# Kernel tuning notes

Hardware: AMD Instinct MI355X
Metric: run time of the kernel (lower is better)

Reference implementation:

```python
import jax, jax.numpy as jnp
import numpy as np

B, T, D = 4, 2048, 1024
H = 16
HD = D // H


def setup_inputs() -> dict:
    key = jax.random.key(0)
    ks = jax.random.split(key, 9)
    s = 1.0 / np.sqrt(D)
    return {
        "x": jax.random.normal(ks[0], (B, T, D), dtype=jnp.float32),
        "Wk": jax.random.normal(ks[1], (D, D), dtype=jnp.float32) * s,
        "bk": jnp.zeros((D,), dtype=jnp.float32),
        "Wq": jax.random.normal(ks[2], (D, D), dtype=jnp.float32) * s,
        "bq": jnp.zeros((D,), dtype=jnp.float32),
        "Wv": jax.random.normal(ks[3], (D, D), dtype=jnp.float32) * s,
        "bv": jnp.zeros((D,), dtype=jnp.float32),
        "Wp": jax.random.normal(ks[4], (D, D), dtype=jnp.float32) * s,
        "bp": jnp.zeros((D,), dtype=jnp.float32),
    }


def reference(x, Wk, bk, Wq, bq, Wv, bv, Wp, bp):
    Bv, Tv, Dv = x.shape
    # project and split heads: [B, H, T, HD]
    def heads(w, b):
        return (x @ w + b).reshape(Bv, Tv, H, HD).transpose(0, 2, 1, 3)
    k = heads(Wk, bk)
    q = heads(Wq, bq)
    v = heads(Wv, bv)
    scale = 1.0 / np.sqrt(HD)
    att = jnp.einsum('bhqd,bhkd->bhqk', q, k) * scale  # [B,H,T,T]
    causal = jnp.tril(jnp.ones((Tv, Tv), dtype=bool))
    att = jnp.where(causal[None, None, :, :], att, -jnp.inf)
    att = jax.nn.softmax(att, axis=-1)
    y = jnp.einsum('bhqk,bhkd->bhqd', att, v)  # [B,H,T,HD]
    y = y.transpose(0, 2, 1, 3).reshape(Bv, Tv, Dv)
    return y @ Wp + bp
```

## Files before the change

kernel.cpp:

```cpp
#include <hip/hip_runtime.h>
#include <stdint.h>

#define Bb 4
#define Tt 2048
#define Dd 1024
#define Hh 16
#define HDd 64
#define Mm 8192

typedef __attribute__((ext_vector_type(8))) short bf16x8;
typedef __attribute__((ext_vector_type(4))) float f32x4;
typedef __attribute__((ext_vector_type(16))) float f32x16;

#define MFMA(a, b, c) __builtin_amdgcn_mfma_f32_16x16x32_bf16(a, b, c, 0, 0, 0)
#define MFMA32(a, b, c) __builtin_amdgcn_mfma_f32_32x32x16_bf16(a, b, c, 0, 0, 0)

#define LOG2E 1.44269504088896340736f
#if __has_builtin(__builtin_amdgcn_exp2f)
#define EXP2(x) __builtin_amdgcn_exp2f(x)
#else
#define EXP2(x) __expf((x) * 0.69314718055994530942f)
#endif

union vfu { uint2 u2[2]; bf16x8 v; };
union apu { uint32_t u[4]; bf16x8 v; };

__device__ __forceinline__ unsigned short f2b(float f) {
  union { float f; uint32_t u; } v; v.f = f;
  return (unsigned short)((v.u + 0x7FFFu + ((v.u >> 16) & 1u)) >> 16);
}

__device__ __forceinline__ uint32_t pk2(float a, float b) {
  union { __bf16 h[2]; uint32_t u; } x;
  x.h[0] = (__bf16)a; x.h[1] = (__bf16)b;
  return x.u;
}

__device__ __forceinline__ void gload_lds16(const void* g, void* l) {
  __builtin_amdgcn_global_load_lds(
      (const __attribute__((address_space(1))) void*)g,
      (__attribute__((address_space(3))) void*)l, 16, 0, 0);
}

__global__ __launch_bounds__(256) void k_convert_x(const float* __restrict__ x,
                                                   unsigned short* __restrict__ xb) {
  int i = (blockIdx.x * 256 + threadIdx.x) * 8;
  float4 a = *(const float4*)(x + i);
  float4 b = *(const float4*)(x + i + 4);
  uint4 o;
  o.x = f2b(a.x) | ((uint32_t)f2b(a.y) << 16);
  o.y = f2b(a.z) | ((uint32_t)f2b(a.w) << 16);
  o.z = f2b(b.x) | ((uint32_t)f2b(b.y) << 16);
  o.w = f2b(b.z) | ((uint32_t)f2b(b.w) << 16);
  *(uint4*)(xb + i) = o;
}

__global__ __launch_bounds__(256) void k_transpose_w(
    const float* __restrict__ Wk, const float* __restrict__ Wq,
    const float* __restrict__ Wv, const float* __restrict__ Wp,
    unsigned short* __restrict__ WkT, unsigned short* __restrict__ WqT,
    unsigned short* __restrict__ WvT, unsigned short* __restrict__ WpT) {
  const float* W; unsigned short* O;
  int wsel = blockIdx.y;
  W = wsel == 0 ? Wk : wsel == 1 ? Wq : wsel == 2 ? Wv : Wp;
  O = wsel == 0 ? WkT : wsel == 1 ? WqT : wsel == 2 ? WvT : WpT;
  __shared__ unsigned short tile[32][36];
  int kb = (blockIdx.x >> 5) << 5;
  int nb = (blockIdx.x & 31) << 5;
  int t = threadIdx.x;
  int r = t >> 3, c4 = (t & 7) << 2;
  float4 v = *(const float4*)(W + (size_t)(kb + r) * Dd + nb + c4);
  tile[r][c4 + 0] = f2b(v.x); tile[r][c4 + 1] = f2b(v.y);
  tile[r][c4 + 2] = f2b(v.z); tile[r][c4 + 3] = f2b(v.w);
  __syncthreads();
  uint2 o;
  o.x = tile[c4 + 0][r] | ((uint32_t)tile[c4 + 1][r] << 16);
  o.y = tile[c4 + 2][r] | ((uint32_t)tile[c4 + 3][r] << 16);
  *(uint2*)(O + (size_t)(nb + r) * Dd + kb + c4) = o;
}

__global__ __launch_bounds__(256, 2) void k_gemm3(
    const unsigned short* __restrict__ A,
    const unsigned short* __restrict__ BtQ, const unsigned short* __restrict__ BtK,
    const unsigned short* __restrict__ BtV,
    const float* __restrict__ bq, const float* __restrict__ bk,
    const float* __restrict__ bv,
    unsigned short* __restrict__ Qb, unsigned short* __restrict__ Kb,
    unsigned short* __restrict__ VTb) {
  __shared__ __align__(16) unsigned short Al[2][128 * 32];
  __shared__ __align__(16) unsigned short Bl[2][3][128 * 32];
  int tid = threadIdx.x;
  int lane = tid & 63, wid = tid >> 6;
  int wr = wid >> 1, wc = wid & 1;
  int lq = lane & 15, lh = lane >> 4;
  int mb = blockIdx.x * 128;
  int nb = blockIdx.y << 7;

  int srow = (wid << 5) + (lane >> 2);
  int scol = (lane & 3) << 3;
  const unsigned short* Ag = A + (size_t)(mb + srow) * Dd + scol;
  const unsigned short* Bg0 = BtQ + (size_t)(nb + srow) * Dd + scol;
  const unsigned short* Bg1 = BtK + (size_t)(nb + srow) * Dd + scol;
  const unsigned short* Bg2 = BtV + (size_t)(nb + srow) * Dd + scol;
  int lofs = wid << 10;

#define STAGE3(kb_, bi_) do {                                            \
    gload_lds16(Ag + (kb_), &Al[bi_][0] + lofs);                         \
    gload_lds16(Ag + (kb_) + 16 * Dd, &Al[bi_][0] + lofs + 16 * 32);     \
    gload_lds16(Bg0 + (kb_), &Bl[bi_][0][0] + lofs);                     \
    gload_lds16(Bg0 + (kb_) + 16 * Dd, &Bl[bi_][0][0] + lofs + 16 * 32); \
    gload_lds16(Bg1 + (kb_), &Bl[bi_][1][0] + lofs);                     \
    gload_lds16(Bg1 + (kb_) + 16 * Dd, &Bl[bi_][1][0] + lofs + 16 * 32); \
    gload_lds16(Bg2 + (kb_), &Bl[bi_][2][0] + lofs);                     \
    gload_lds16(Bg2 + (kb_) + 16 * Dd, &Bl[bi_][2][0] + lofs + 16 * 32); \
  } while (0)

  f32x4 zero = {0.f, 0.f, 0.f, 0.f};
  f32x4 acc[3][4][4];
#pragma unroll
  for (int s = 0; s < 3; s++)
#pragma unroll
    for (int m = 0; m < 4; m++)
#pragma unroll
      for (int n = 0; n < 4; n++) acc[s][m][n] = zero;

  STAGE3(0, 0);
  __syncthreads();

  int cur = 0;
  for (int kb = 0; kb < Dd; kb += 32) {
    if (kb + 32 < Dd) STAGE3(kb + 32, cur ^ 1);
    bf16x8 af[4];
#pragma unroll
    for (int m = 0; m < 4; m++)
      af[m] = *(const bf16x8*)(&Al[cur][0] +
                               (((wr << 6) + (m << 4) + lq) << 5) + (lh << 3));
#pragma unroll
    for (int s = 0; s < 3; s++) {
      bf16x8 bf[4];
#pragma unroll
      for (int n = 0; n < 4; n++)
        bf[n] = *(const bf16x8*)(&Bl[cur][s][0] +
                                 (((wc << 6) + (n << 4) + lq) << 5) + (lh << 3));
      __builtin_amdgcn_s_setprio(1);
#pragma unroll
      for (int m = 0; m < 4; m++)
#pragma unroll
        for (int n = 0; n < 4; n++) acc[s][m][n] = MFMA(af[m], bf[n], acc[s][m][n]);
      __builtin_amdgcn_s_setprio(0);
    }
    __syncthreads();
    cur ^= 1;
  }
#undef STAGE3

  int b_idx = mb >> 11;
#pragma unroll
  for (int s = 0; s < 3; s++) {
#pragma unroll
    for (int n = 0; n < 4; n++) {
      int col = nb + (wc << 6) + (n << 4) + lq;
      float bbias = (s == 0) ? bq[col] : (s == 1) ? bk[col] : bv[col];
      int hh = col >> 6, hd = col & 63;
#pragma unroll
      for (int m = 0; m < 4; m++) {
        int row0 = mb + (wr << 6) + (m << 4) + (lh << 2);
        int t0 = row0 & 2047;
        if (s == 2) {
          float v0 = acc[s][m][n][0] + bbias, v1 = acc[s][m][n][1] + bbias;
          float v2 = acc[s][m][n][2] + bbias, v3 = acc[s][m][n][3] + bbias;
          uint2 pv;
          pv.x = f2b(v0) | ((uint32_t)f2b(v1) << 16);
          pv.y = f2b(v2) | ((uint32_t)f2b(v3) << 16);
          int t0s = t0 ^ ((hd & 7) << 3);
          *(uint2*)(VTb + ((size_t)(b_idx * 16 + hh) * 64 + hd) * Tt + t0s) = pv;
        } else {
          unsigned short* O = (s == 0) ? Qb : Kb;
          float sc = (s == 0) ? (0.125f * LOG2E) : 1.0f;
#pragma unroll
          for (int r = 0; r < 4; r++) {
            float v = (acc[s][m][n][r] + bbias) * sc;
            int trow = t0 + r;
            int hds = (s == 0) ? hd : (hd ^ ((trow & 7) << 3));
            O[((size_t)(b_idx * 16 + hh) * Tt + trow) * 64 + hds] = f2b(v);
          }
        }
      }
    }
  }
}

__global__ __launch_bounds__(256) void k_gemm(
    const unsigned short* __restrict__ A,
    const unsigned short* __restrict__ Bt0,
    const float* __restrict__ bias0,
    float* __restrict__ Pout) {
  __shared__ __align__(16) unsigned short Al[2][128 * 32];
  __shared__ __align__(16) unsigned short Bl[2][128 * 32];
  int tid = threadIdx.x;
  int lane = tid & 63, wid = tid >> 6;
  int wr = wid >> 1, wc = wid & 1;
  int lq = lane & 15, lh = lane >> 4;
  int mb = blockIdx.x * 128;
  int nb = blockIdx.y << 7;

  int srow = (wid << 5) + (lane >> 2);
  int scol = (lane & 3) << 3;
  const unsigned short* Ag = A + (size_t)(mb + srow) * Dd + scol;
  const unsigned short* Bg = Bt0 + (size_t)(nb + srow) * Dd + scol;
  int lofs = wid << 10;

#define STAGEP(kb_, bi_) do {                                            \
    gload_lds16(Ag + (kb_), &Al[bi_][0] + lofs);                         \
    gload_lds16(Ag + (kb_) + 16 * Dd, &Al[bi_][0] + lofs + 16 * 32);     \
    gload_lds16(Bg + (kb_), &Bl[bi_][0] + lofs);                         \
    gload_lds16(Bg + (kb_) + 16 * Dd, &Bl[bi_][0] + lofs + 16 * 32);     \
  } while (0)

  f32x4 zero = {0.f, 0.f, 0.f, 0.f};
  f32x4 acc[4][4];
#pragma unroll
  for (int m = 0; m < 4; m++)
#pragma unroll
    for (int n = 0; n < 4; n++) acc[m][n] = zero;

  STAGEP(0, 0);
  __syncthreads();

  int cur = 0;
  for (int kb = 0; kb < Dd; kb += 32) {
    if (kb + 32 < Dd) STAGEP(kb + 32, cur ^ 1);
    bf16x8 af[4], bf[4];
#pragma unroll
    for (int m = 0; m < 4; m++)
      af[m] = *(const bf16x8*)(&Al[cur][0] +
                               (((wr << 6) + (m << 4) + lq) << 5) + (lh << 3));
#pragma unroll
    for (int n = 0; n < 4; n++)
      bf[n] = *(const bf16x8*)(&Bl[cur][0] +
                               (((wc << 6) + (n << 4) + lq) << 5) + (lh << 3));
    __builtin_amdgcn_s_setprio(1);
#pragma unroll
    for (int m = 0; m < 4; m++)
#pragma unroll
      for (int n = 0; n < 4; n++) acc[m][n] = MFMA(af[m], bf[n], acc[m][n]);
    __builtin_amdgcn_s_setprio(0);
    __syncthreads();
    cur ^= 1;
  }
#undef STAGEP

#pragma unroll
  for (int n = 0; n < 4; n++) {
    int col = nb + (wc << 6) + (n << 4) + lq;
    float bb = bias0[col];
#pragma unroll
    for (int m = 0; m < 4; m++) {
      int row0 = mb + (wr << 6) + (m << 4) + (lh << 2);
#pragma unroll
      for (int r = 0; r < 4; r++)
        Pout[(size_t)(row0 + r) * Dd + col] = acc[m][n][r] + bb;
    }
  }
}

__global__ __launch_bounds__(256, 2) void k_attn(
    const unsigned short* __restrict__ Qb, const unsigned short* __restrict__ Kb,
    const unsigned short* __restrict__ VTb, unsigned short* __restrict__ yb) {
  __shared__ __align__(16) unsigned short KL[2][8192];
  __shared__ __align__(16) unsigned short VL[2][8192];
  int b = blockIdx.x;
  int qt = (b < 256) ? (7 - (b >> 6)) : ((b - 256) >> 6);
  int rr6 = b & 63;
  int bh = ((rr6 & 7) << 3) | (rr6 >> 3);
  int tid = threadIdx.x, lane = tid & 63, w = tid >> 6;
  int l31 = lane & 31, hi = lane >> 5;
  const unsigned short* __restrict__ Qh = Qb + (size_t)bh * Tt * 64;
  const unsigned short* __restrict__ Kh = Kb + (size_t)bh * Tt * 64;
  const unsigned short* __restrict__ Vh = VTb + (size_t)bh * 64 * Tt;
  int qgA = (qt << 8) + (w << 6);
  int qgB = qgA + 32;

  bf16x8 qfA[4], qfB[4];
#pragma unroll
  for (int c = 0; c < 4; c++) {
    qfA[c] = *(const bf16x8*)(Qh + (size_t)(qgA + l31) * 64 + (c << 4) + (hi << 3));
    qfB[c] = *(const bf16x8*)(Qh + (size_t)(qgB + l31) * 64 + (c << 4) + (hi << 3));
  }

  f32x16 accA0, accA1, accB0, accB1, accLA, accLB;
#pragma unroll
  for (int i = 0; i < 16; i++) {
    accA0[i] = 0.f; accA1[i] = 0.f; accB0[i] = 0.f; accB1[i] = 0.f;
    accLA[i] = 0.f; accLB[i] = 0.f;
  }
  apu onesf;
  onesf.u[0] = onesf.u[1] = onesf.u[2] = onesf.u[3] = 0x3F803F80u;

  int jmaxb = (qt << 1) + 1;
  int srowK = lane >> 3, scolK = (lane & 7) << 3;
  int rowbK = w << 5;
  int srowV = lane >> 4, scolV = (lane & 15) << 3;
  int rowbV = w << 4;
  int swz = l31 & 7;

#define STAGE(kvt_, bi_) do {                                                        \
    int kv_ = (kvt_) << 7;                                                           \
    gload_lds16(Kh + (size_t)(kv_ + rowbK + srowK) * 64 + scolK,                     \
                &KL[bi_][rowbK << 6]);                                               \
    gload_lds16(Kh + (size_t)(kv_ + rowbK + 8 + srowK) * 64 + scolK,                 \
                &KL[bi_][(rowbK + 8) << 6]);                                         \
    gload_lds16(Kh + (size_t)(kv_ + rowbK + 16 + srowK) * 64 + scolK,                \
                &KL[bi_][(rowbK + 16) << 6]);                                        \
    gload_lds16(Kh + (size_t)(kv_ + rowbK + 24 + srowK) * 64 + scolK,                \
                &KL[bi_][(rowbK + 24) << 6]);                                        \
    gload_lds16(Vh + (size_t)(rowbV + srowV) * Tt + kv_ + scolV,                     \
                &VL[bi_][rowbV << 7]);                                               \
    gload_lds16(Vh + (size_t)(rowbV + 4 + srowV) * Tt + kv_ + scolV,                 \
                &VL[bi_][(rowbV + 4) << 7]);                                         \
    gload_lds16(Vh + (size_t)(rowbV + 8 + srowV) * Tt + kv_ + scolV,                 \
                &VL[bi_][(rowbV + 8) << 7]);                                         \
    gload_lds16(Vh + (size_t)(rowbV + 12 + srowV) * Tt + kv_ + scolV,                \
                &VL[bi_][(rowbV + 12) << 7]);                                        \
  } while (0)

  STAGE(0, 0);
  __syncthreads();

  int cur = 0;
  for (int jt = 0; jt <= jmaxb; ++jt) {
    if (jt < jmaxb) STAGE(jt + 1, cur ^ 1);
    int base_kv = jt << 7;
    if (qgB >= base_kv) {
      const unsigned short* KB = &KL[cur][0];
      const unsigned short* VB = &VL[cur][0];
#pragma unroll
      for (int n2 = 0; n2 < 4; n2++) {
        int rel_base = qgA - base_kv - (n2 << 5);
        if (rel_base >= -32) {
          bool doA = (rel_base >= 0);
          bf16x8 kf[4];
          int krowb = ((n2 << 5) + l31) << 6;
#pragma unroll
          for (int c = 0; c < 4; c++)
            kf[c] = *(const bf16x8*)(KB + krowb + ((((c << 1) + hi) ^ swz) << 3));
          f32x16 sA, sB;
#pragma unroll
          for (int i = 0; i < 16; i++) { sA[i] = 0.f; sB[i] = 0.f; }
          __builtin_amdgcn_s_setprio(1);
          if (doA) {
#pragma unroll
            for (int c = 0; c < 4; c++) {
              sA = MFMA32(kf[c], qfA[c], sA);
              sB = MFMA32(kf[c], qfB[c], sB);
            }
          } else {
#pragma unroll
            for (int c = 0; c < 4; c++) sB = MFMA32(kf[c], qfB[c], sB);
          }
          __builtin_amdgcn_s_setprio(0);
          float pA[16], pB[16];
          if (rel_base <= 0) {
            int relA = rel_base + l31, relB = relA + 32;
#pragma unroll
            for (int r = 0; r < 16; r++) {
              int krow = (r & 3) + ((r >> 2) << 3) + (hi << 2);
              if (doA) pA[r] = EXP2(krow > relA ? -1e30f : sA[r]);
              pB[r] = EXP2(krow > relB ? -1e30f : sB[r]);
            }
          } else {
#pragma unroll
            for (int r = 0; r < 16; r++) { pA[r] = EXP2(sA[r]); pB[r] = EXP2(sB[r]); }
          }
          vfu vf[2][2];
#pragma unroll
          for (int n2v = 0; n2v < 2; n2v++) {
            int vrowb = ((n2v << 5) + l31) << 7;
#pragma unroll
            for (int cc = 0; cc < 2; cc++) {
              int blk0 = (n2 << 2) + (cc << 1);
              vf[n2v][cc].u2[0] =
                  *(const uint2*)(VB + vrowb + ((blk0 ^ swz) << 3) + (hi << 2));
              vf[n2v][cc].u2[1] =
                  *(const uint2*)(VB + vrowb + (((blk0 + 1) ^ swz) << 3) + (hi << 2));
            }
          }
          apu b0, b1;
#pragma unroll
          for (int g = 0; g < 4; g++) {
            b0.u[g] = pk2(pB[2 * g], pB[2 * g + 1]);
            b1.u[g] = pk2(pB[8 + 2 * g], pB[8 + 2 * g + 1]);
          }
          __builtin_amdgcn_s_setprio(1);
          accB0 = MFMA32(b0.v, vf[0][0].v, accB0);
          accB1 = MFMA32(b0.v, vf[1][0].v, accB1);
          accLB = MFMA32(b0.v, onesf.v, accLB);
          accB0 = MFMA32(b1.v, vf[0][1].v, accB0);
          accB1 = MFMA32(b1.v, vf[1][1].v, accB1);
          accLB = MFMA32(b1.v, onesf.v, accLB);
          __builtin_amdgcn_s_setprio(0);
          if (doA) {
            apu a0, a1;
#pragma unroll
            for (int g = 0; g < 4; g++) {
              a0.u[g] = pk2(pA[2 * g], pA[2 * g + 1]);
              a1.u[g] = pk2(pA[8 + 2 * g], pA[8 + 2 * g + 1]);
            }
            __builtin_amdgcn_s_setprio(1);
            accA0 = MFMA32(a0.v, vf[0][0].v, accA0);
            accA1 = MFMA32(a0.v, vf[1][0].v, accA1);
            accLA = MFMA32(a0.v, onesf.v, accLA);
            accA0 = MFMA32(a1.v, vf[0][1].v, accA0);
            accA1 = MFMA32(a1.v, vf[1][1].v, accA1);
            accLA = MFMA32(a1.v, onesf.v, accLA);
            __builtin_amdgcn_s_setprio(0);
          }
        }
      }
    }
    __syncthreads();
    cur ^= 1;
  }
#undef STAGE

  int bb = bh >> 4, hh = bh & 15;
#pragma unroll
  for (int r = 0; r < 16; r++) {
    int qr = (r & 3) + ((r >> 2) << 3) + (hi << 2);
    float invqA = 1.0f / accLA[r];
    float invqB = 1.0f / accLB[r];
    size_t baseA = ((size_t)(bb * Tt + qgA + qr)) * Dd + (hh << 6) + l31;
    size_t baseB = ((size_t)(bb * Tt + qgB + qr)) * Dd + (hh << 6) + l31;
    yb[baseA] = f2b(accA0[r] * invqA);
    yb[baseA + 32] = f2b(accA1[r] * invqA);
    yb[baseB] = f2b(accB0[r] * invqB);
    yb[baseB + 32] = f2b(accB1[r] * invqB);
  }
}

extern "C" void kernel_launch(void* const* d_in, const int* in_sizes, int n_in,
                              void* d_out, int out_size, void* d_ws, size_t ws_size,
                              hipStream_t stream) {
  const float* x = (const float*)d_in[0];
  const float* Wk = (const float*)d_in[1];
  const float* bk = (const float*)d_in[2];
  const float* Wq = (const float*)d_in[3];
  const float* bq = (const float*)d_in[4];
  const float* Wv = (const float*)d_in[5];
  const float* bv = (const float*)d_in[6];
  const float* Wp = (const float*)d_in[7];
  const float* bp = (const float*)d_in[8];
  float* out = (float*)d_out;

  char* ws = (char*)d_ws;
  unsigned short* xb  = (unsigned short*)(ws);
  unsigned short* WkT = (unsigned short*)(ws + (16ull << 20));
  unsigned short* WqT = (unsigned short*)(ws + (18ull << 20));
  unsigned short* WvT = (unsigned short*)(ws + (20ull << 20));
  unsigned short* WpT = (unsigned short*)(ws + (22ull << 20));
  unsigned short* Qb  = (unsigned short*)(ws + (24ull << 20));
  unsigned short* Kb  = (unsigned short*)(ws + (40ull << 20));
  unsigned short* VTb = (unsigned short*)(ws + (56ull << 20));
  unsigned short* yb  = (unsigned short*)(ws + (72ull << 20));

  k_convert_x<<<4096, 256, 0, stream>>>(x, xb);
  k_transpose_w<<<dim3(1024, 4), 256, 0, stream>>>(Wk, Wq, Wv, Wp, WkT, WqT, WvT, WpT);
  k_gemm3<<<dim3(64, 8), 256, 0, stream>>>(xb, WqT, WkT, WvT, bq, bk, bv,
                                           Qb, Kb, VTb);
  k_attn<<<512, 256, 0, stream>>>(Qb, Kb, VTb, yb);
  k_gemm<<<dim3(64, 8), 256, 0, stream>>>(yb, WpT, bp, out);
}
```

Baseline: 160.7 us.

## Pair low and high causal query tiles per block to balance attention work

Each block now processes two 128-row query halves, one from the front of the sequence and one from the back (tile p and tile 15-p), instead of a contiguous 256-row query tile. The combined causal work per block is therefore nearly constant, removing the load imbalance between early and late query tiles and the old heavy-first scheduling order. The masking logic is rewritten to handle the two tiles' diagonals separately. The cost is that every block iterates over KV tiles up to the larger tile's diagonal, and the A half skips MFMAs once it passes its own diagonal.

```diff
diff --git a/kernel.cpp b/kernel.cpp
--- a/kernel.cpp
+++ b/kernel.cpp
@@ -270,7 +270,7 @@
   __shared__ __align__(16) unsigned short KL[2][8192];
   __shared__ __align__(16) unsigned short VL[2][8192];
   int b = blockIdx.x;
-  int qt = (b < 256) ? (7 - (b >> 6)) : ((b - 256) >> 6);
+  int p = b >> 6;
   int rr6 = b & 63;
   int bh = ((rr6 & 7) << 3) | (rr6 >> 3);
   int tid = threadIdx.x, lane = tid & 63, w = tid >> 6;
@@ -278,8 +278,8 @@
   const unsigned short* __restrict__ Qh = Qb + (size_t)bh * Tt * 64;
   const unsigned short* __restrict__ Kh = Kb + (size_t)bh * Tt * 64;
   const unsigned short* __restrict__ Vh = VTb + (size_t)bh * 64 * Tt;
-  int qgA = (qt << 8) + (w << 6);
-  int qgB = qgA + 32;
+  int qgA = (p << 7) + (w << 5);
+  int qgB = ((15 - p) << 7) + (w << 5);
 
   bf16x8 qfA[4], qfB[4];
 #pragma unroll
@@ -297,7 +297,7 @@
   apu onesf;
   onesf.u[0] = onesf.u[1] = onesf.u[2] = onesf.u[3] = 0x3F803F80u;
 
-  int jmaxb = (qt << 1) + 1;
+  int jmaxb = 15 - p;
   int srowK = lane >> 3, scolK = (lane & 7) << 3;
   int rowbK = w << 5;
   int srowV = lane >> 4, scolV = (lane & 15) << 3;
@@ -331,90 +331,101 @@
   for (int jt = 0; jt <= jmaxb; ++jt) {
     if (jt < jmaxb) STAGE(jt + 1, cur ^ 1);
     int base_kv = jt << 7;
-    if (qgB >= base_kv) {
-      const unsigned short* KB = &KL[cur][0];
-      const unsigned short* VB = &VL[cur][0];
-#pragma unroll
-      for (int n2 = 0; n2 < 4; n2++) {
-        int rel_base = qgA - base_kv - (n2 << 5);
-        if (rel_base >= -32) {
-          bool doA = (rel_base >= 0);
-          bf16x8 kf[4];
-          int krowb = ((n2 << 5) + l31) << 6;
-#pragma unroll
-          for (int c = 0; c < 4; c++)
-            kf[c] = *(const bf16x8*)(KB + krowb + ((((c << 1) + hi) ^ swz) << 3));
-          f32x16 sA, sB;
-#pragma unroll
-          for (int i = 0; i < 16; i++) { sA[i] = 0.f; sB[i] = 0.f; }
-          __builtin_amdgcn_s_setprio(1);
-          if (doA) {
-#pragma unroll
-            for (int c = 0; c < 4; c++) {
-              sA = MFMA32(kf[c], qfA[c], sA);
-              sB = MFMA32(kf[c], qfB[c], sB);
+    const unsigned short* KB = &KL[cur][0];
+    const unsigned short* VB = &VL[cur][0];
+#pragma unroll
+    for (int n2 = 0; n2 < 4; n2++) {
+      int relB = qgB - base_kv - (n2 << 5);
+      int relA = qgA - base_kv - (n2 << 5);
+      if (relB >= 0) {
+        bool doA = (relA >= 0);
+        bf16x8 kf[4];
+        int krowb = ((n2 << 5) + l31) << 6;
+#pragma unroll
+        for (int c = 0; c < 4; c++)
+          kf[c] = *(const bf16x8*)(KB + krowb + ((((c << 1) + hi) ^ swz) << 3));
+        f32x16 sA, sB;
+#pragma unroll
+        for (int i = 0; i < 16; i++) { sA[i] = 0.f; sB[i] = 0.f; }
+        __builtin_amdgcn_s_setprio(1);
+        if (doA) {
+#pragma unroll
+          for (int c = 0; c < 4; c++) {
+            sA = MFMA32(kf[c], qfA[c], sA);
+            sB = MFMA32(kf[c], qfB[c], sB);
+          }
+        } else {
+#pragma unroll
+          for (int c = 0; c < 4; c++) sB = MFMA32(kf[c], qfB[c], sB);
+        }
+        __builtin_amdgcn_s_setprio(0);
+        float pA[16], pB[16];
+        if (relB == 0) {
+          int rB = l31;
+#pragma unroll
+          for (int r = 0; r < 16; r++) {
+            int krow = (r & 3) + ((r >> 2) << 3) + (hi << 2);
+            pB[r] = EXP2(krow > rB ? -1e30f : sB[r]);
+          }
+        } else {
+#pragma unroll
+          for (int r = 0; r < 16; r++) pB[r] = EXP2(sB[r]);
+        }
+        if (doA) {
+          if (relA == 0) {
+            int rA = l31;
+#pragma unroll
+            for (int r = 0; r < 16; r++) {
+              int krow = (r & 3) + ((r >> 2) << 3) + (hi << 2);
+              pA[r] = EXP2(krow > rA ? -1e30f : sA[r]);
             }
           } else {
 #pragma unroll
-            for (int c = 0; c < 4; c++) sB = MFMA32(kf[c], qfB[c], sB);
-          }
+            for (int r = 0; r < 16; r++) pA[r] = EXP2(sA[r]);
+          }
+        }
+        vfu vf[2][2];
+#pragma unroll
+        for (int n2v = 0; n2v < 2; n2v++) {
+          int vrowb = ((n2v << 5) + l31) << 7;
+#pragma unroll
+          for (int cc = 0; cc < 2; cc++) {
+            int blk0 = (n2 << 2) + (cc << 1);
+            vf[n2v][cc].u2[0] =
+                *(const uint2*)(VB + vrowb + ((blk0 ^ swz) << 3) + (hi << 2));
+            vf[n2v][cc].u2[1] =
+                *(const uint2*)(VB + vrowb + (((blk0 + 1) ^ swz) << 3) + (hi << 2));
+          }
+        }
+        apu b0, b1;
+#pragma unroll
+        for (int g = 0; g < 4; g++) {
+          b0.u[g] = pk2(pB[2 * g], pB[2 * g + 1]);
+          b1.u[g] = pk2(pB[8 + 2 * g], pB[8 + 2 * g + 1]);
+        }
+        __builtin_amdgcn_s_setprio(1);
+        accB0 = MFMA32(b0.v, vf[0][0].v, accB0);
+        accB1 = MFMA32(b0.v, vf[1][0].v, accB1);
+        accLB = MFMA32(b0.v, onesf.v, accLB);
+        accB0 = MFMA32(b1.v, vf[0][1].v, accB0);
+        accB1 = MFMA32(b1.v, vf[1][1].v, accB1);
+        accLB = MFMA32(b1.v, onesf.v, accLB);
+        __builtin_amdgcn_s_setprio(0);
+        if (doA) {
+          apu a0, a1;
+#pragma unroll
+          for (int g = 0; g < 4; g++) {
+            a0.u[g] = pk2(pA[2 * g], pA[2 * g + 1]);
+            a1.u[g] = pk2(pA[8 + 2 * g], pA[8 + 2 * g + 1]);
+          }
+          __builtin_amdgcn_s_setprio(1);
+          accA0 = MFMA32(a0.v, vf[0][0].v, accA0);
+          accA1 = MFMA32(a0.v, vf[1][0].v, accA1);
+          accLA = MFMA32(a0.v, onesf.v, accLA);
+          accA0 = MFMA32(a1.v, vf[0][1].v, accA0);
+          accA1 = MFMA32(a1.v, vf[1][1].v, accA1);
+          accLA = MFMA32(a1.v, onesf.v, accLA);
           __builtin_amdgcn_s_setprio(0);
-          float pA[16], pB[16];
-          if (rel_base <= 0) {
-            int relA = rel_base + l31, relB = relA + 32;
-#pragma unroll
-            for (int r = 0; r < 16; r++) {
-              int krow = (r & 3) + ((r >> 2) << 3) + (hi << 2);
-              if (doA) pA[r] = EXP2(krow > relA ? -1e30f : sA[r]);
-              pB[r] = EXP2(krow > relB ? -1e30f : sB[r]);
-            }
-          } else {
-#pragma unroll
-            for (int r = 0; r < 16; r++) { pA[r] = EXP2(sA[r]); pB[r] = EXP2(sB[r]); }
-          }
-          vfu vf[2][2];
-#pragma unroll
-          for (int n2v = 0; n2v < 2; n2v++) {
-            int vrowb = ((n2v << 5) + l31) << 7;
-#pragma unroll
-            for (int cc = 0; cc < 2; cc++) {
-              int blk0 = (n2 << 2) + (cc << 1);
-              vf[n2v][cc].u2[0] =
-                  *(const uint2*)(VB + vrowb + ((blk0 ^ swz) << 3) + (hi << 2));
-              vf[n2v][cc].u2[1] =
-                  *(const uint2*)(VB + vrowb + (((blk0 + 1) ^ swz) << 3) + (hi << 2));
-            }
-          }
-          apu b0, b1;
-#pragma unroll
-          for (int g = 0; g < 4; g++) {
-            b0.u[g] = pk2(pB[2 * g], pB[2 * g + 1]);
-            b1.u[g] = pk2(pB[8 + 2 * g], pB[8 + 2 * g + 1]);
-          }
-          __builtin_amdgcn_s_setprio(1);
-          accB0 = MFMA32(b0.v, vf[0][0].v, accB0);
-          accB1 = MFMA32(b0.v, vf[1][0].v, accB1);
-          accLB = MFMA32(b0.v, onesf.v, accLB);
-          accB0 = MFMA32(b1.v, vf[0][1].v, accB0);
-          accB1 = MFMA32(b1.v, vf[1][1].v, accB1);
-          accLB = MFMA32(b1.v, onesf.v, accLB);
-          __builtin_amdgcn_s_setprio(0);
-          if (doA) {
-            apu a0, a1;
-#pragma unroll
-            for (int g = 0; g < 4; g++) {
-              a0.u[g] = pk2(pA[2 * g], pA[2 * g + 1]);
-              a1.u[g] = pk2(pA[8 + 2 * g], pA[8 + 2 * g + 1]);
-            }
-            __builtin_amdgcn_s_setprio(1);
-            accA0 = MFMA32(a0.v, vf[0][0].v, accA0);
-            accA1 = MFMA32(a0.v, vf[1][0].v, accA1);
-            accLA = MFMA32(a0.v, onesf.v, accLA);
-            accA0 = MFMA32(a1.v, vf[0][1].v, accA0);
-            accA1 = MFMA32(a1.v, vf[1][1].v, accA1);
-            accLA = MFMA32(a1.v, onesf.v, accLA);
-            __builtin_amdgcn_s_setprio(0);
-          }
         }
       }
     }
```

Result: faster. 153.3 us (median of 2 runs) (-4.6%).
